# Kernel tuning notes

Hardware: AMD Instinct MI355X
Metric: run time of the kernel (lower is better)

Reference implementation:

```python
import jax, jax.numpy as jnp
import numpy as np

B, S, D = 2, 2048, 1024
H = 16
HD = D // H
MLP = 4096
EPS = 1e-5


def _layernorm(x, g, b):
    mu = jnp.mean(x, axis=-1, keepdims=True)
    var = jnp.mean(jnp.square(x - mu), axis=-1, keepdims=True)
    return (x - mu) * jax.lax.rsqrt(var + EPS) * g + b


def setup_inputs() -> dict:
    key = jax.random.key(0)
    ks = jax.random.split(key, 16)
    sd = 0.02
    return {
        "x": jax.random.normal(ks[0], (B, S, D), jnp.float32),
        "dis_attn_mask": jax.random.normal(ks[1], (B, S, S), jnp.float32) * 0.1,
        "cls_attn_mask": jax.random.normal(ks[2], (B, S, S), jnp.float32) * 0.1,
        "wq": jax.random.normal(ks[3], (D, D), jnp.float32) * sd,
        "bq": jnp.zeros((D,), jnp.float32),
        "wk": jax.random.normal(ks[4], (D, D), jnp.float32) * sd,
        "bk": jnp.zeros((D,), jnp.float32),
        "wv": jax.random.normal(ks[5], (D, D), jnp.float32) * sd,
        "bv": jnp.zeros((D,), jnp.float32),
        "ln1_g": jnp.ones((D,), jnp.float32),
        "ln1_b": jnp.zeros((D,), jnp.float32),
        "ln2_g": jnp.ones((D,), jnp.float32),
        "ln2_b": jnp.zeros((D,), jnp.float32),
        "w1": jax.random.normal(ks[6], (D, MLP), jnp.float32) * sd,
        "b1": jnp.zeros((MLP,), jnp.float32),
        "w2": jax.random.normal(ks[7], (MLP, D), jnp.float32) * sd,
        "b2": jnp.zeros((D,), jnp.float32),
    }


def reference(x, dis_attn_mask, cls_attn_mask, wq, bq, wk, bk, wv, bv,
              ln1_g, ln1_b, ln2_g, ln2_b, w1, b1, w2, b2):
    res = x
    h = _layernorm(x, ln1_g, ln1_b)
    q = h @ wq + bq
    k = h @ wk + bk
    v = h @ wv + bv
    # NOTE: original torch code uses .view(B, H, S, HD) on a contiguous
    # [B, S, D] tensor (no transpose); row-major reshape reproduces this.
    q = q.reshape(B, H, S, HD)
    k = k.reshape(B, H, S, HD)
    v = v.reshape(B, H, S, HD)
    w = jnp.einsum('bhsd,bhtd->bhst', q, k) * (HD ** -0.5)
    w = w + dis_attn_mask[:, None] + cls_attn_mask[:, None]
    w = jax.nn.softmax(w, axis=-1)
    h_attn = jnp.einsum('bhst,bhtd->bhsd', w, v).reshape(B, S, D)
    h = h_attn + res
    h = _layernorm(h, ln2_g, ln2_b)
    res2 = h
    h = jax.nn.gelu(h @ w1 + b1, approximate=False) @ w2 + b2
    return h + res2
```

## Files before the change

### kernel.cpp

```cpp
#include <hip/hip_runtime.h>
#include <hip/hip_bf16.h>
#include <math.h>

#define BB 2
#define SS 2048
#define DD 1024
#define HH 16
#define MLPD 4096

typedef __attribute__((ext_vector_type(8))) short bf16x8;
typedef __attribute__((ext_vector_type(4))) float f32x4;
typedef __attribute__((ext_vector_type(4))) unsigned short us4;

static __device__ __forceinline__ float fast_exp2(float x) {
#if __has_builtin(__builtin_amdgcn_exp2f)
  return __builtin_amdgcn_exp2f(x);
#else
  return exp2f(x);
#endif
}
static __device__ __forceinline__ float fast_rcp(float x) {
#if __has_builtin(__builtin_amdgcn_rcpf)
  return __builtin_amdgcn_rcpf(x);
#else
  return 1.0f / x;
#endif
}

static __device__ __forceinline__ unsigned short f2bf(float f) {
  union { float f; unsigned int u; } v; v.f = f;
  unsigned int r = v.u + 0x7fffu + ((v.u >> 16) & 1u);
  return (unsigned short)(r >> 16);
}
static __device__ __forceinline__ float bf2f(unsigned short b) {
  return __uint_as_float(((unsigned int)b) << 16);
}

static __device__ __forceinline__ float gelu_f(float x) {
  float u = x * x;
  float z = x * fmaf(u, 0.0713548162f, 1.59576912f);
  float e = fast_exp2(z * -1.44269504f);
  return x * fast_rcp(1.0f + e);
}

static __device__ __forceinline__ int swz(int row) {
  return (row & 3) ^ ((row >> 2) & 3);
}

static __device__ __forceinline__ void async16(const unsigned short* g, unsigned short* l) {
  __builtin_amdgcn_global_load_lds(
      (const __attribute__((address_space(1))) unsigned int*)g,
      (__attribute__((address_space(3))) unsigned int*)l, 16, 0, 0);
}

__global__ __launch_bounds__(256) void transpose_to_bf16(
    const float* __restrict__ src, unsigned short* __restrict__ dst,
    int K, int N) {
  __shared__ float tile[32][33];
  int t = threadIdx.x;
  int c = t & 31, rl = t >> 5;
  int bx = blockIdx.x, by = blockIdx.y;
#pragma unroll
  for (int i = 0; i < 4; ++i) {
    int row = rl * 4 + i;
    tile[row][c] = src[(size_t)(by * 32 + row) * N + bx * 32 + c];
  }
  __syncthreads();
#pragma unroll
  for (int i = 0; i < 4; ++i) {
    int n = rl * 4 + i;
    dst[(size_t)(bx * 32 + n) * K + by * 32 + c] = f2bf(tile[c][n]);
  }
}

__global__ __launch_bounds__(256) void transpose_qkv(
    const float* __restrict__ wq, const float* __restrict__ wk,
    const float* __restrict__ wv, unsigned short* __restrict__ dst) {
  __shared__ float tile[32][33];
  const float* src = blockIdx.z == 0 ? wq : blockIdx.z == 1 ? wk : wv;
  unsigned short* d = dst + (size_t)blockIdx.z * 1024 * 1024;
  int t = threadIdx.x;
  int c = t & 31, rl = t >> 5;
  int bx = blockIdx.x, by = blockIdx.y;
#pragma unroll
  for (int i = 0; i < 4; ++i) {
    int row = rl * 4 + i;
    tile[row][c] = src[(size_t)(by * 32 + row) * DD + bx * 32 + c];
  }
  __syncthreads();
#pragma unroll
  for (int i = 0; i < 4; ++i) {
    int n = rl * 4 + i;
    d[(size_t)(bx * 32 + n) * DD + by * 32 + c] = f2bf(tile[c][n]);
  }
}

__global__ __launch_bounds__(256) void concat_bias(
    const float* __restrict__ bq, const float* __restrict__ bk,
    const float* __restrict__ bv, float* __restrict__ dst) {
  int i = blockIdx.x * 256 + threadIdx.x;
  if (i < 1024) dst[i] = bq[i];
  else if (i < 2048) dst[i] = bk[i - 1024];
  else if (i < 3072) dst[i] = bv[i - 2048];
}

__global__ __launch_bounds__(256) void mask_prep3(
    const float* __restrict__ dis, const float* __restrict__ cls,
    unsigned short* __restrict__ cmP) {
  __shared__ unsigned short sm[16][512];
  int qtO = blockIdx.x, waveO = blockIdx.y;
  int b = blockIdx.z >> 2, ktg = blockIdx.z & 3;
  int t = threadIdx.x;
  int row0 = qtO * 128 + waveO * 16;
  int col0 = ktg * 512;
  const float* db = dis + (size_t)b * SS * SS;
  const float* cb = cls + (size_t)b * SS * SS;
  int lrow = t >> 4, lcg = t & 15;
#pragma unroll
  for (int shot = 0; shot < 8; ++shot) {
    int cc = lcg * 4 + shot * 64;
    size_t idx = (size_t)(row0 + lrow) * SS + col0 + cc;
    float4 d4 = *(const float4*)(db + idx);
    float4 c4 = *(const float4*)(cb + idx);
    us4 o;
    o[0] = f2bf((d4.x + c4.x) * 8.0f);
    o[1] = f2bf((d4.y + c4.y) * 8.0f);
    o[2] = f2bf((d4.z + c4.z) * 8.0f);
    o[3] = f2bf((d4.w + c4.w) * 8.0f);
    *(us4*)&sm[lrow][cc] = o;
  }
  __syncthreads();
  int ktL = t >> 5, lp = t & 31;
  unsigned short* ob =
      cmP + ((((size_t)b * 16 + qtO) * 8 + waveO) * 32 + ktg * 8 + ktL) * 64 * 16;
#pragma unroll
  for (int li = 0; li < 2; ++li) {
    int l = lp * 2 + li;
    int g = l >> 4, c16 = l & 15;
    short v[16];
#pragma unroll
    for (int t4 = 0; t4 < 4; ++t4)
#pragma unroll
      for (int r = 0; r < 4; ++r)
        v[t4 * 4 + r] = (short)sm[g * 4 + r][ktL * 64 + t4 * 16 + c16];
    unsigned short* o = ob + (size_t)l * 16;
    *(bf16x8*)(o) = *(bf16x8*)&v[0];
    *(bf16x8*)(o + 8) = *(bf16x8*)&v[8];
  }
}

template <bool BF_IN, bool ADD>
__global__ __launch_bounds__(256) void ln_bf16(
    const void* __restrict__ in, const float* __restrict__ add,
    const float* __restrict__ g, const float* __restrict__ beta,
    unsigned short* __restrict__ out) {
  int row = blockIdx.x;
  int t = threadIdx.x;
  float x[4];
  if (BF_IN) {
    us4 b4 = *(const us4*)((const unsigned short*)in + (size_t)row * DD + t * 4);
#pragma unroll
    for (int i = 0; i < 4; ++i) x[i] = bf2f(b4[i]);
  } else {
    float4 f4 = *(const float4*)((const float*)in + (size_t)row * DD + t * 4);
    x[0] = f4.x; x[1] = f4.y; x[2] = f4.z; x[3] = f4.w;
  }
  if (ADD) {
    float4 a4 = *(const float4*)(add + (size_t)row * DD + t * 4);
    x[0] += a4.x; x[1] += a4.y; x[2] += a4.z; x[3] += a4.w;
  }
  float s1 = x[0] + x[1] + x[2] + x[3];
  float s2 = x[0] * x[0] + x[1] * x[1] + x[2] * x[2] + x[3] * x[3];
#pragma unroll
  for (int off = 32; off > 0; off >>= 1) {
    s1 += __shfl_down(s1, off);
    s2 += __shfl_down(s2, off);
  }
  __shared__ float sa[4], sb[4];
  int wid = t >> 6;
  if ((t & 63) == 0) { sa[wid] = s1; sb[wid] = s2; }
  __syncthreads();
  s1 = sa[0] + sa[1] + sa[2] + sa[3];
  s2 = sb[0] + sb[1] + sb[2] + sb[3];
  float mean = s1 * (1.0f / 1024.0f);
  float var = s2 * (1.0f / 1024.0f) - mean * mean;
  float rstd = rsqrtf(var + 1e-5f);
  float4 gv = *(const float4*)(g + t * 4);
  float4 bv = *(const float4*)(beta + t * 4);
  us4 o;
  o[0] = f2bf((x[0] - mean) * rstd * gv.x + bv.x);
  o[1] = f2bf((x[1] - mean) * rstd * gv.y + bv.y);
  o[2] = f2bf((x[2] - mean) * rstd * gv.z + bv.z);
  o[3] = f2bf((x[3] - mean) * rstd * gv.w + bv.w);
  *(us4*)(out + (size_t)row * DD + t * 4) = o;
}

template <int BN, bool GELU, bool ADDSRC, bool OUT_BF16, bool SPLIT3>
__global__ __launch_bounds__(256) void gemm_bf16(
    const unsigned short* __restrict__ A, const unsigned short* __restrict__ BT,
    const float* __restrict__ bias, const unsigned short* __restrict__ addsrc,
    void* C0, void* C1, void* C2, int M, int N, int K) {
  constexpr int BJ = BN / 32;
  constexpr int BCH = BN / 64;
  __shared__ __align__(16) unsigned short As[128][32];
  __shared__ __align__(16) unsigned short Bs[BN][32];
  int tid = threadIdx.x;
  int wave = tid >> 6, lane = tid & 63;
  int g = lane >> 4, c16 = lane & 15;
  int nwg = gridDim.x * gridDim.y;
  int wg = blockIdx.y * gridDim.x + blockIdx.x;
  int cpx = nwg >> 3;
  int sw = (wg & 7) * cpx + (wg >> 3);
  int bxs = sw % gridDim.x, bys = sw / gridDim.x;
  int m0 = bys * 128, n0 = bxs * BN;
  int wm = (wave >> 1) * 64, wn = (wave & 1) * (BN / 2);
  int lrow = lane >> 2, lq = lane & 3;
  int dq = (lq ^ swz(lrow)) * 8;
  const unsigned short* aS = A + (size_t)(m0 + wave * 32 + lrow) * K + lq * 8;
  unsigned short* aD0 = &As[wave * 32 + lrow][dq];
  unsigned short* aD1 = &As[wave * 32 + 16 + lrow][dq];
  const unsigned short* bS = BT + (size_t)(n0 + wave * (BCH * 16) + lrow) * K + lq * 8;
  unsigned short* bD0 = &Bs[wave * (BCH * 16) + lrow][dq];
  unsigned short* bD1 = &Bs[(wave * (BCH * 16) + 16 + lrow) % BN][dq];
  int vA = (g ^ swz(c16)) * 8;
  const int KI = K / 32;
  const size_t rK = 16 * (size_t)K;

  bf16x8 a0a = *(const bf16x8*)(aS);
  bf16x8 a1a = *(const bf16x8*)(aS + rK);
  bf16x8 b0a = *(const bf16x8*)(bS);
  bf16x8 b1a;
  if constexpr (BCH == 2) b1a = *(const bf16x8*)(bS + rK);
  bf16x8 a0b = *(const bf16x8*)(aS + 32);
  bf16x8 a1b = *(const bf16x8*)(aS + rK + 32);
  bf16x8 b0b = *(const bf16x8*)(bS + 32);
  bf16x8 b1b;
  if constexpr (BCH == 2) b1b = *(const bf16x8*)(bS + rK + 32);

  f32x4 acc[4][BJ] = {};
  for (int kt = 0; kt < KI; kt += 2) {
    __syncthreads();
    *(bf16x8*)aD0 = a0a;
    *(bf16x8*)aD1 = a1a;
    *(bf16x8*)bD0 = b0a;
    if constexpr (BCH == 2) *(bf16x8*)bD1 = b1a;
    __syncthreads();
    if (kt + 2 < KI) {
      int ko = (kt + 2) * 32;
      a0a = *(const bf16x8*)(aS + ko);
      a1a = *(const bf16x8*)(aS + rK + ko);
      b0a = *(const bf16x8*)(bS + ko);
      if constexpr (BCH == 2) b1a = *(const bf16x8*)(bS + rK + ko);
    }
    {
      bf16x8 a[4], b[BJ];
#pragma unroll
      for (int i = 0; i < 4; ++i) a[i] = *(const bf16x8*)&As[wm + i * 16 + c16][vA];
#pragma unroll
      for (int j = 0; j < BJ; ++j) b[j] = *(const bf16x8*)&Bs[wn + j * 16 + c16][vA];
#pragma unroll
      for (int i = 0; i < 4; ++i)
#pragma unroll
        for (int j = 0; j < BJ; ++j)
          acc[i][j] = __builtin_amdgcn_mfma_f32_16x16x32_bf16(a[i], b[j], acc[i][j], 0, 0, 0);
    }
    __syncthreads();
    *(bf16x8*)aD0 = a0b;
    *(bf16x8*)aD1 = a1b;
    *(bf16x8*)bD0 = b0b;
    if constexpr (BCH == 2) *(bf16x8*)bD1 = b1b;
    __syncthreads();
    if (kt + 3 < KI) {
      int ko = (kt + 3) * 32;
      a0b = *(const bf16x8*)(aS + ko);
      a1b = *(const bf16x8*)(aS + rK + ko);
      b0b = *(const bf16x8*)(bS + ko);
      if constexpr (BCH == 2) b1b = *(const bf16x8*)(bS + rK + ko);
    }
    {
      bf16x8 a[4], b[BJ];
#pragma unroll
      for (int i = 0; i < 4; ++i) a[i] = *(const bf16x8*)&As[wm + i * 16 + c16][vA];
#pragma unroll
      for (int j = 0; j < BJ; ++j) b[j] = *(const bf16x8*)&Bs[wn + j * 16 + c16][vA];
#pragma unroll
      for (int i = 0; i < 4; ++i)
#pragma unroll
        for (int j = 0; j < BJ; ++j)
          acc[i][j] = __builtin_amdgcn_mfma_f32_16x16x32_bf16(a[i], b[j], acc[i][j], 0, 0, 0);
    }
  }
  unsigned short* dstb = nullptr;
  int lc0 = 0;
  if (SPLIT3) {
    int which = n0 >> 10;
    dstb = (unsigned short*)(which == 0 ? C0 : which == 1 ? C1 : C2);
    lc0 = n0 & 1023;
  }
#pragma unroll
  for (int j = 0; j < BJ; ++j) {
    int coff = wn + j * 16 + c16;
    float bj = bias[n0 + coff];
#pragma unroll
    for (int i = 0; i < 4; ++i) {
#pragma unroll
      for (int r = 0; r < 4; ++r) {
        int row = m0 + wm + i * 16 + g * 4 + r;
        float cval = acc[i][j][r] + bj;
        if (GELU) cval = gelu_f(cval);
        if (ADDSRC) cval += bf2f(addsrc[(size_t)row * N + n0 + coff]);
        if (SPLIT3) {
          dstb[(size_t)row * 1024 + lc0 + coff] = f2bf(cval);
        } else if (OUT_BF16) {
          ((unsigned short*)C0)[(size_t)row * N + n0 + coff] = f2bf(cval);
        } else {
          ((float*)C0)[(size_t)row * N + n0 + coff] = cval;
        }
      }
    }
  }
}

#define VMW(n) asm volatile("s_waitcnt vmcnt(" #n ")" ::: "memory")
#define BARX() do { asm volatile("" ::: "memory"); \
                    __builtin_amdgcn_s_barrier(); \
                    asm volatile("" ::: "memory"); } while (0)

template <bool GELU, bool SPLIT3>
__global__ __launch_bounds__(512, 2) void gemm256(
    const unsigned short* __restrict__ A, const unsigned short* __restrict__ BT,
    const float* __restrict__ bias, void* C0, void* C1, void* C2,
    int N, int K) {
  __shared__ __align__(16) char lds[2][2][2][16384];
  int tid = threadIdx.x;
  int lane = tid & 63, w = tid >> 6;
  int g = lane >> 4, c16 = lane & 15;
  int wm16 = (w >> 2) << 4;
  int wn16 = (w & 3) << 4;
  int nwg = gridDim.x * gridDim.y;
  int wg = blockIdx.y * gridDim.x + blockIdx.x;
  int cpx = nwg >> 3;
  int sw = (wg & 7) * cpx + (wg >> 3);
  int bx = sw % gridDim.x, by = sw / gridDim.x;
  int m0 = by << 8, n0 = bx << 8;

  int st0 = tid >> 6, ci0 = tid & 63;
  int cp0 = ci0 ^ (((ci0 >> 5) & 1) << 1);
  int sr0 = ((st0 >> 1) << 4) + (cp0 >> 2);
  int sk0 = ((st0 & 1) << 5) + ((cp0 & 3) << 3);
  size_t soff = (size_t)sr0 * K + sk0;

  auto stage = [&](int op, int h, int tt, int d) {
    const unsigned short* base = (op == 0 ? A : BT);
    int row0 = (op == 0 ? m0 : n0) + (h << 7);
    const unsigned short* src = base + (size_t)row0 * K + (tt << 6) + soff;
    unsigned short* dst = (unsigned short*)&lds[op][d][h][tid * 16];
    async16(src, dst);
    async16(src + ((size_t)K << 6), dst + 4096);
  };

  auto foff = [&](int r, int ke) -> int {
    int stt = ((r >> 4) << 1) + (ke >> 5);
    int loc = ((r & 15) << 6) + ((ke & 31) << 1);
    return (stt << 10) + (loc ^ (((r >> 3) & 1) << 5));
  };
  int offA[4][2], offB[2][2];
#pragma unroll
  for (int ii = 0; ii < 4; ++ii)
#pragma unroll
    for (int ks = 0; ks < 2; ++ks)
      offA[ii][ks] = foff(ii * 32 + wm16 + c16, ks * 32 + g * 8);
#pragma unroll
  for (int jj = 0; jj < 2; ++jj)
#pragma unroll
    for (int ks = 0; ks < 2; ++ks)
      offB[jj][ks] = foff(jj * 64 + wn16 + c16, ks * 32 + g * 8);

  f32x4 acc[8][4] = {};

#define MFMA_Q(IH, JH, AF, BF) do {                                           \
    __builtin_amdgcn_s_setprio(1);                                            \
    _Pragma("unroll") for (int ii = 0; ii < 4; ++ii)                          \
      _Pragma("unroll") for (int jj = 0; jj < 2; ++jj) {                      \
        acc[(IH)*4+ii][(JH)*2+jj] = __builtin_amdgcn_mfma_f32_16x16x32_bf16(  \
            AF[ii][0], BF[jj][0], acc[(IH)*4+ii][(JH)*2+jj], 0, 0, 0);        \
        acc[(IH)*4+ii][(JH)*2+jj] = __builtin_amdgcn_mfma_f32_16x16x32_bf16(  \
            AF[ii][1], BF[jj][1], acc[(IH)*4+ii][(JH)*2+jj], 0, 0, 0);        \
      }                                                                       \
    __builtin_amdgcn_s_setprio(0);                                            \
  } while (0)

  stage(0, 0, 0, 0);
  stage(1, 0, 0, 0);
  stage(0, 1, 0, 0);
  stage(1, 1, 0, 0);
  VMW(4);
  BARX();

  const int KT = K >> 6;
  for (int kt = 0; kt < KT; ++kt) {
    int d = kt & 1, dn = d ^ 1;
    int t1 = kt + 1 < KT ? kt + 1 : KT - 1;
    const char* pd = &lds[0][d][0][0];
    bf16x8 A0f[4][2], A1f[4][2], Bf[2][2];

#pragma unroll
    for (int ii = 0; ii < 4; ++ii)
#pragma unroll
      for (int ks = 0; ks < 2; ++ks)
        A0f[ii][ks] = *(const bf16x8*)(pd + offA[ii][ks]);
#pragma unroll
    for (int jj = 0; jj < 2; ++jj)
#pragma unroll
      for (int ks = 0; ks < 2; ++ks)
        Bf[jj][ks] = *(const bf16x8*)(pd + 65536 + offB[jj][ks]);
    stage(0, 0, t1, dn);
    stage(1, 0, t1, dn);
    VMW(6);
    BARX();
    MFMA_Q(0, 0, A0f, Bf);
    BARX();

#pragma unroll
    for (int ii = 0; ii < 4; ++ii)
#pragma unroll
      for (int ks = 0; ks < 2; ++ks)
        A1f[ii][ks] = *(const bf16x8*)(pd + 16384 + offA[ii][ks]);
    stage(0, 1, t1, dn);
    VMW(6);
    BARX();
    MFMA_Q(1, 0, A1f, Bf);
    BARX();

#pragma unroll
    for (int jj = 0; jj < 2; ++jj)
#pragma unroll
      for (int ks = 0; ks < 2; ++ks)
        Bf[jj][ks] = *(const bf16x8*)(pd + 81920 + offB[jj][ks]);
    stage(1, 1, t1, dn);
    BARX();
    MFMA_Q(1, 1, A1f, Bf);
    BARX();

    VMW(4);
    BARX();
    MFMA_Q(0, 1, A0f, Bf);
    BARX();
  }
#undef MFMA_Q
  VMW(0);

  unsigned short* dstb = nullptr;
  int lc0 = 0;
  if (SPLIT3) {
    int which = n0 >> 10;
    dstb = (unsigned short*)(which == 0 ? C0 : which == 1 ? C1 : C2);
    lc0 = n0 & 1023;
  }
#pragma unroll
  for (int i = 0; i < 8; ++i) {
#pragma unroll
    for (int j = 0; j < 4; ++j) {
      int row_b = m0 + ((i >> 2) << 7) + ((i & 3) << 5) + wm16 + (g << 2);
      int colp = ((j >> 1) << 7) + ((j & 1) << 6) + wn16 + c16;
      float bj = bias[n0 + colp];
#pragma unroll
      for (int r = 0; r < 4; ++r) {
        float cv = acc[i][j][r] + bj;
        if (GELU) cv = gelu_f(cv);
        int row = row_b + r;
        if (SPLIT3) {
          dstb[(size_t)row * 1024 + lc0 + colp] = f2bf(cv);
        } else {
          ((unsigned short*)C0)[(size_t)row * N + n0 + colp] = f2bf(cv);
        }
      }
    }
  }
}

__global__ __launch_bounds__(512) void attn_mfma256(
    const unsigned short* __restrict__ q, const unsigned short* __restrict__ k,
    const unsigned short* __restrict__ v, const unsigned short* __restrict__ cmP,
    unsigned short* __restrict__ outO) {
  __shared__ __align__(16) unsigned short Ks[2][64][32];
  __shared__ __align__(16) unsigned short Vt[64][72];
  __shared__ __align__(16) unsigned short Ps[256][72];
  int tid = threadIdx.x;
  int wave = tid >> 6, lane = tid & 63;
  int g = lane >> 4, c16 = lane & 15;
  int w = blockIdx.x + 8 * blockIdx.y + 128 * blockIdx.z;
  int qt = (w >> 4) & 7;
  int b = (w >> 3) & 1;
  int h = (w & 7) | (((w >> 7) & 1) << 3);
  int s0 = qt * 256;
  int wr = wave * 32;
  size_t headoff = (size_t)b * SS * DD + (size_t)h * SS * 64;
  const unsigned short* qb = q + headoff;
  const unsigned short* kb = k + headoff;
  const unsigned short* vb = v + headoff;
  int qtA = qt * 2 + (wave >> 2);
  int wOA = (wave & 3) * 2;
  const unsigned short* csrcA =
      cmP + ((((size_t)b * 16 + qtA) * 8 + wOA) * 2048 + lane) * 16;
  const unsigned short* csrcB = csrcA + 2048 * 16;

  int kkey = tid >> 3, kseg = tid & 7;
  unsigned short* kdst = &Ks[kseg >> 2][kkey][((kseg & 3) ^ swz(kkey)) * 8];
  const unsigned short* ksrc = kb + (size_t)kkey * 64 + kseg * 8;
  const unsigned short* vsrc = vb + (size_t)lane * 64 + wave * 8;
  int vK = (g ^ swz(c16)) * 8;

  bf16x8 qf0A, qf1A, qf0B, qf1B;
  {
    size_t qrowA = (size_t)(s0 + wr + c16) * 64;
    size_t qrowB = (size_t)(s0 + wr + 16 + c16) * 64;
    qf0A = *(const bf16x8*)(qb + qrowA + g * 8);
    qf1A = *(const bf16x8*)(qb + qrowA + 32 + g * 8);
    qf0B = *(const bf16x8*)(qb + qrowB + g * 8);
    qf1B = *(const bf16x8*)(qb + qrowB + 32 + g * 8);
  }
  bf16x8 ones;
#pragma unroll
  for (int j = 0; j < 8; ++j) ones[j] = (short)0x3F80;
  f32x4 oA[4] = {}, oB[4] = {};
  f32x4 olA = {}, olB = {};
  const float scale2 = 0.18033688f;

  bf16x8 kreg = *(const bf16x8*)(ksrc);
  bf16x8 vreg = *(const bf16x8*)(vsrc);
  bf16x8 cmA0 = *(const bf16x8*)(csrcA);
  bf16x8 cmA1 = *(const bf16x8*)(csrcA + 8);
  bf16x8 cmB0 = *(const bf16x8*)(csrcB);
  bf16x8 cmB1 = *(const bf16x8*)(csrcB + 8);

  for (int kt = 0; kt < 32; ++kt) {
    __syncthreads();
    *(bf16x8*)kdst = kreg;
#pragma unroll
    for (int j = 0; j < 8; ++j) Vt[wave * 8 + j][lane] = (unsigned short)vreg[j];
    __syncthreads();

    int ktn = kt + 1 < 32 ? kt + 1 : 31;
    bf16x8 kregN = *(const bf16x8*)(ksrc + (size_t)ktn * 4096);
    bf16x8 vregN = *(const bf16x8*)(vsrc + (size_t)ktn * 4096);
    bf16x8 cmA0N = *(const bf16x8*)(csrcA + (size_t)ktn * 1024);
    bf16x8 cmA1N = *(const bf16x8*)(csrcA + (size_t)ktn * 1024 + 8);
    bf16x8 cmB0N = *(const bf16x8*)(csrcB + (size_t)ktn * 1024);
    bf16x8 cmB1N = *(const bf16x8*)(csrcB + (size_t)ktn * 1024 + 8);

    f32x4 sA[4], sB[4];
#pragma unroll
    for (int r = 0; r < 4; ++r) {
      sA[0][r] = bf2f((unsigned short)cmA0[r]);
      sA[1][r] = bf2f((unsigned short)cmA0[4 + r]);
      sA[2][r] = bf2f((unsigned short)cmA1[r]);
      sA[3][r] = bf2f((unsigned short)cmA1[4 + r]);
      sB[0][r] = bf2f((unsigned short)cmB0[r]);
      sB[1][r] = bf2f((unsigned short)cmB0[4 + r]);
      sB[2][r] = bf2f((unsigned short)cmB1[r]);
      sB[3][r] = bf2f((unsigned short)cmB1[4 + r]);
    }
#pragma unroll
    for (int t = 0; t < 4; ++t) {
      bf16x8 b0 = *(const bf16x8*)&Ks[0][t * 16 + c16][vK];
      bf16x8 b1 = *(const bf16x8*)&Ks[1][t * 16 + c16][vK];
      sA[t] = __builtin_amdgcn_mfma_f32_16x16x32_bf16(qf0A, b0, sA[t], 0, 0, 0);
      sA[t] = __builtin_amdgcn_mfma_f32_16x16x32_bf16(qf1A, b1, sA[t], 0, 0, 0);
      sB[t] = __builtin_amdgcn_mfma_f32_16x16x32_bf16(qf0B, b0, sB[t], 0, 0, 0);
      sB[t] = __builtin_amdgcn_mfma_f32_16x16x32_bf16(qf1B, b1, sB[t], 0, 0, 0);
    }
#pragma unroll
    for (int t = 0; t < 4; ++t) {
      int colw = ((t + g) & 3) * 16 + c16;
#pragma unroll
      for (int r = 0; r < 4; ++r) {
        float pA = fast_exp2(sA[t][r] * scale2);
        Ps[wr + g * 4 + r][colw] = (unsigned short)(__float_as_uint(pA) >> 16);
        float pB = fast_exp2(sB[t][r] * scale2);
        Ps[wr + 16 + g * 4 + r][colw] = (unsigned short)(__float_as_uint(pB) >> 16);
      }
    }
#pragma unroll
    for (int ks = 0; ks < 2; ++ks) {
      int ttc = ((ks * 2 + (g >> 1)) + ((c16 >> 2) & 3)) & 3;
      int colp = ttc * 16 + (g & 1) * 8;
      bf16x8 paA = *(const bf16x8*)&Ps[wr + c16][colp];
      bf16x8 paB = *(const bf16x8*)&Ps[wr + 16 + c16][colp];
#pragma unroll
      for (int t2 = 0; t2 < 4; ++t2) {
        bf16x8 vb8 = *(const bf16x8*)&Vt[t2 * 16 + c16][ks * 32 + g * 8];
        oA[t2] = __builtin_amdgcn_mfma_f32_16x16x32_bf16(paA, vb8, oA[t2], 0, 0, 0);
        oB[t2] = __builtin_amdgcn_mfma_f32_16x16x32_bf16(paB, vb8, oB[t2], 0, 0, 0);
      }
      olA = __builtin_amdgcn_mfma_f32_16x16x32_bf16(paA, ones, olA, 0, 0, 0);
      olB = __builtin_amdgcn_mfma_f32_16x16x32_bf16(paB, ones, olB, 0, 0, 0);
    }
    kreg = kregN;
    vreg = vregN;
    cmA0 = cmA0N; cmA1 = cmA1N;
    cmB0 = cmB0N; cmB1 = cmB1N;
  }
  float invA[4], invB[4];
#pragma unroll
  for (int r = 0; r < 4; ++r) {
    invA[r] = fast_rcp(olA[r]);
    invB[r] = fast_rcp(olB[r]);
  }
#pragma unroll
  for (int t2 = 0; t2 < 4; ++t2)
#pragma unroll
    for (int r = 0; r < 4; ++r) {
      int srowA = s0 + wr + g * 4 + r;
      int srowB = srowA + 16;
      outO[headoff + (size_t)srowA * 64 + t2 * 16 + c16] = f2bf(oA[t2][r] * invA[r]);
      outO[headoff + (size_t)srowB * 64 + t2 * 16 + c16] = f2bf(oB[t2][r] * invB[r]);
    }
}

extern "C" void kernel_launch(void* const* d_in, const int* in_sizes, int n_in,
                              void* d_out, int out_size, void* d_ws, size_t ws_size,
                              hipStream_t stream) {
  const float* x    = (const float*)d_in[0];
  const float* dis  = (const float*)d_in[1];
  const float* cls  = (const float*)d_in[2];
  const float* wq   = (const float*)d_in[3];
  const float* bq   = (const float*)d_in[4];
  const float* wk   = (const float*)d_in[5];
  const float* bk   = (const float*)d_in[6];
  const float* wv   = (const float*)d_in[7];
  const float* bv   = (const float*)d_in[8];
  const float* ln1g = (const float*)d_in[9];
  const float* ln1b = (const float*)d_in[10];
  const float* ln2g = (const float*)d_in[11];
  const float* ln2b = (const float*)d_in[12];
  const float* w1   = (const float*)d_in[13];
  const float* b1   = (const float*)d_in[14];
  const float* w2   = (const float*)d_in[15];
  const float* b2   = (const float*)d_in[16];
  float* out = (float*)d_out;
  char* ws = (char*)d_ws;

  unsigned short* qkvwT = (unsigned short*)(ws + 0);
  unsigned short* w1T   = (unsigned short*)(ws + 6291456);
  unsigned short* w2T   = (unsigned short*)(ws + 14680064);
  float*          qkvb  = (float*)(ws + 23068672);
  unsigned short* r1    = (unsigned short*)(ws + 23134208);
  unsigned short* qbuf  = (unsigned short*)(ws + 31522816);
  unsigned short* kbuf  = (unsigned short*)(ws + 39911424);
  unsigned short* vbuf  = (unsigned short*)(ws + 48300032);
  unsigned short* h2    = (unsigned short*)(ws + 56688640);
  unsigned short* cmP   = (unsigned short*)(ws + 65077248);
  unsigned short* mm    = (unsigned short*)(ws + 23134208);
  unsigned short* h1 = r1;
  unsigned short* attnO = r1;

  const int rows = BB * SS;

  transpose_qkv<<<dim3(DD / 32, DD / 32, 3), 256, 0, stream>>>(wq, wk, wv, qkvwT);
  transpose_to_bf16<<<dim3(MLPD / 32, DD / 32), 256, 0, stream>>>(w1, w1T, DD, MLPD);
  transpose_to_bf16<<<dim3(DD / 32, MLPD / 32), 256, 0, stream>>>(w2, w2T, MLPD, DD);
  concat_bias<<<12, 256, 0, stream>>>(bq, bk, bv, qkvb);
  mask_prep3<<<dim3(16, 8, 8), 256, 0, stream>>>(dis, cls, cmP);

  ln_bf16<false, false><<<rows, 256, 0, stream>>>(x, nullptr, ln1g, ln1b, h1);

  gemm256<false, true><<<dim3(3072 / 256, rows / 256), 512, 0, stream>>>(
      h1, qkvwT, qkvb, qbuf, kbuf, vbuf, 3072, DD);

  attn_mfma256<<<dim3(SS / 256, HH, BB), 512, 0, stream>>>(
      qbuf, kbuf, vbuf, cmP, attnO);

  ln_bf16<true, true><<<rows, 256, 0, stream>>>(attnO, x, ln2g, ln2b, h2);

  gemm256<true, false><<<dim3(MLPD / 256, rows / 256), 512, 0, stream>>>(
      h2, w1T, b1, mm, nullptr, nullptr, MLPD, DD);

  gemm_bf16<64, false, true, false, false><<<dim3(DD / 64, rows / 128), 256, 0, stream>>>(
      mm, w2T, b2, h2, out, nullptr, nullptr, rows, DD, MLPD);
}
```

Measured before the change: 388.4 us.

## Fuse prep kernels into one launch and keep attention P in registers

Merges LN1, the three weight transposes, bias concat and mask packing into a single prep_all launch to cut launch overhead and let independent work overlap. The attention kernel is rewritten to compute S transposed (K as the A operand), so exp results stay in registers and feed the PV MFMA directly, removing the Ps shared-memory round trip. Blocks shrink to 256 threads with 128 query rows each, and the mask layout is adjusted to match. Outputs are written as vectorized us4 stores. Risks are register pressure and a changed V/mask layout that must line up exactly with the new MFMA fragment mapping.

```diff
diff --git a/kernel.cpp b/kernel.cpp
--- a/kernel.cpp
+++ b/kernel.cpp
@@ -35,6 +35,9 @@
 static __device__ __forceinline__ float bf2f(unsigned short b) {
   return __uint_as_float(((unsigned int)b) << 16);
 }
+static __device__ __forceinline__ unsigned int packbf(float lo, float hi) {
+  return (__float_as_uint(lo) >> 16) | (__float_as_uint(hi) & 0xFFFF0000u);
+}
 
 static __device__ __forceinline__ float gelu_f(float x) {
   float u = x * x;
@@ -53,99 +56,147 @@
       (__attribute__((address_space(3))) unsigned int*)l, 16, 0, 0);
 }
 
-__global__ __launch_bounds__(256) void transpose_to_bf16(
-    const float* __restrict__ src, unsigned short* __restrict__ dst,
-    int K, int N) {
-  __shared__ float tile[32][33];
+__global__ __launch_bounds__(256) void prep_all(
+    const float* __restrict__ x, const float* __restrict__ ln1g,
+    const float* __restrict__ ln1b, unsigned short* __restrict__ h1,
+    const float* __restrict__ wq, const float* __restrict__ wk,
+    const float* __restrict__ wv, unsigned short* __restrict__ qkvwT,
+    const float* __restrict__ w1, unsigned short* __restrict__ w1T,
+    const float* __restrict__ w2, unsigned short* __restrict__ w2T,
+    const float* __restrict__ dis, const float* __restrict__ cls,
+    unsigned short* __restrict__ cmP,
+    const float* __restrict__ bq, const float* __restrict__ bk,
+    const float* __restrict__ bv, float* __restrict__ qkvb) {
+  __shared__ __align__(16) char smraw[16384];
+  int bid = blockIdx.x;
   int t = threadIdx.x;
-  int c = t & 31, rl = t >> 5;
-  int bx = blockIdx.x, by = blockIdx.y;
-#pragma unroll
-  for (int i = 0; i < 4; ++i) {
-    int row = rl * 4 + i;
-    tile[row][c] = src[(size_t)(by * 32 + row) * N + bx * 32 + c];
-  }
-  __syncthreads();
-#pragma unroll
-  for (int i = 0; i < 4; ++i) {
-    int n = rl * 4 + i;
-    dst[(size_t)(bx * 32 + n) * K + by * 32 + c] = f2bf(tile[c][n]);
-  }
-}
-
-__global__ __launch_bounds__(256) void transpose_qkv(
-    const float* __restrict__ wq, const float* __restrict__ wk,
-    const float* __restrict__ wv, unsigned short* __restrict__ dst) {
-  __shared__ float tile[32][33];
-  const float* src = blockIdx.z == 0 ? wq : blockIdx.z == 1 ? wk : wv;
-  unsigned short* d = dst + (size_t)blockIdx.z * 1024 * 1024;
-  int t = threadIdx.x;
-  int c = t & 31, rl = t >> 5;
-  int bx = blockIdx.x, by = blockIdx.y;
-#pragma unroll
-  for (int i = 0; i < 4; ++i) {
-    int row = rl * 4 + i;
-    tile[row][c] = src[(size_t)(by * 32 + row) * DD + bx * 32 + c];
-  }
-  __syncthreads();
-#pragma unroll
-  for (int i = 0; i < 4; ++i) {
-    int n = rl * 4 + i;
-    d[(size_t)(bx * 32 + n) * DD + by * 32 + c] = f2bf(tile[c][n]);
-  }
-}
-
-__global__ __launch_bounds__(256) void concat_bias(
-    const float* __restrict__ bq, const float* __restrict__ bk,
-    const float* __restrict__ bv, float* __restrict__ dst) {
-  int i = blockIdx.x * 256 + threadIdx.x;
-  if (i < 1024) dst[i] = bq[i];
-  else if (i < 2048) dst[i] = bk[i - 1024];
-  else if (i < 3072) dst[i] = bv[i - 2048];
-}
-
-__global__ __launch_bounds__(256) void mask_prep3(
-    const float* __restrict__ dis, const float* __restrict__ cls,
-    unsigned short* __restrict__ cmP) {
-  __shared__ unsigned short sm[16][512];
-  int qtO = blockIdx.x, waveO = blockIdx.y;
-  int b = blockIdx.z >> 2, ktg = blockIdx.z & 3;
-  int t = threadIdx.x;
-  int row0 = qtO * 128 + waveO * 16;
-  int col0 = ktg * 512;
-  const float* db = dis + (size_t)b * SS * SS;
-  const float* cb = cls + (size_t)b * SS * SS;
-  int lrow = t >> 4, lcg = t & 15;
-#pragma unroll
-  for (int shot = 0; shot < 8; ++shot) {
-    int cc = lcg * 4 + shot * 64;
-    size_t idx = (size_t)(row0 + lrow) * SS + col0 + cc;
-    float4 d4 = *(const float4*)(db + idx);
-    float4 c4 = *(const float4*)(cb + idx);
+  if (bid < 4096) {
+    int row = bid;
+    float xv[4];
+    float4 f4 = *(const float4*)(x + (size_t)row * DD + t * 4);
+    xv[0] = f4.x; xv[1] = f4.y; xv[2] = f4.z; xv[3] = f4.w;
+    float s1 = xv[0] + xv[1] + xv[2] + xv[3];
+    float s2 = xv[0]*xv[0] + xv[1]*xv[1] + xv[2]*xv[2] + xv[3]*xv[3];
+#pragma unroll
+    for (int off = 32; off > 0; off >>= 1) {
+      s1 += __shfl_down(s1, off);
+      s2 += __shfl_down(s2, off);
+    }
+    float* sa = (float*)smraw;
+    float* sb = sa + 8;
+    int wid = t >> 6;
+    if ((t & 63) == 0) { sa[wid] = s1; sb[wid] = s2; }
+    __syncthreads();
+    s1 = sa[0] + sa[1] + sa[2] + sa[3];
+    s2 = sb[0] + sb[1] + sb[2] + sb[3];
+    float mean = s1 * (1.0f / 1024.0f);
+    float var = s2 * (1.0f / 1024.0f) - mean * mean;
+    float rstd = rsqrtf(var + 1e-5f);
+    float4 gv = *(const float4*)(ln1g + t * 4);
+    float4 bv4 = *(const float4*)(ln1b + t * 4);
     us4 o;
-    o[0] = f2bf((d4.x + c4.x) * 8.0f);
-    o[1] = f2bf((d4.y + c4.y) * 8.0f);
-    o[2] = f2bf((d4.z + c4.z) * 8.0f);
-    o[3] = f2bf((d4.w + c4.w) * 8.0f);
-    *(us4*)&sm[lrow][cc] = o;
-  }
-  __syncthreads();
-  int ktL = t >> 5, lp = t & 31;
-  unsigned short* ob =
-      cmP + ((((size_t)b * 16 + qtO) * 8 + waveO) * 32 + ktg * 8 + ktL) * 64 * 16;
-#pragma unroll
-  for (int li = 0; li < 2; ++li) {
-    int l = lp * 2 + li;
-    int g = l >> 4, c16 = l & 15;
-    short v[16];
-#pragma unroll
-    for (int t4 = 0; t4 < 4; ++t4)
-#pragma unroll
-      for (int r = 0; r < 4; ++r)
-        v[t4 * 4 + r] = (short)sm[g * 4 + r][ktL * 64 + t4 * 16 + c16];
-    unsigned short* o = ob + (size_t)l * 16;
-    *(bf16x8*)(o) = *(bf16x8*)&v[0];
-    *(bf16x8*)(o + 8) = *(bf16x8*)&v[8];
+    o[0] = f2bf((xv[0] - mean) * rstd * gv.x + bv4.x);
+    o[1] = f2bf((xv[1] - mean) * rstd * gv.y + bv4.y);
+    o[2] = f2bf((xv[2] - mean) * rstd * gv.z + bv4.z);
+    o[3] = f2bf((xv[3] - mean) * rstd * gv.w + bv4.w);
+    *(us4*)(h1 + (size_t)row * DD + t * 4) = o;
+  } else if (bid < 4096 + 3072) {
+    int id = bid - 4096;
+    int z = id >> 10;
+    int rem = id & 1023;
+    int bx = rem & 31, by = rem >> 5;
+    const float* src = z == 0 ? wq : z == 1 ? wk : wv;
+    unsigned short* d = qkvwT + (size_t)z * 1024 * 1024;
+    float (*tile)[33] = (float (*)[33])smraw;
+    int c = t & 31, rl = t >> 5;
+#pragma unroll
+    for (int i = 0; i < 4; ++i) {
+      int row = rl * 4 + i;
+      tile[row][c] = src[(size_t)(by * 32 + row) * DD + bx * 32 + c];
+    }
+    __syncthreads();
+#pragma unroll
+    for (int i = 0; i < 4; ++i) {
+      int n = rl * 4 + i;
+      d[(size_t)(bx * 32 + n) * DD + by * 32 + c] = f2bf(tile[c][n]);
+    }
+  } else if (bid < 4096 + 3072 + 4096) {
+    int id = bid - (4096 + 3072);
+    int bx = id & 127, by = id >> 7;
+    float (*tile)[33] = (float (*)[33])smraw;
+    int c = t & 31, rl = t >> 5;
+#pragma unroll
+    for (int i = 0; i < 4; ++i) {
+      int row = rl * 4 + i;
+      tile[row][c] = w1[(size_t)(by * 32 + row) * MLPD + bx * 32 + c];
+    }
+    __syncthreads();
+#pragma unroll
+    for (int i = 0; i < 4; ++i) {
+      int n = rl * 4 + i;
+      w1T[(size_t)(bx * 32 + n) * DD + by * 32 + c] = f2bf(tile[c][n]);
+    }
+  } else if (bid < 4096 + 3072 + 4096 + 4096) {
+    int id = bid - (4096 + 3072 + 4096);
+    int bx = id & 31, by = id >> 5;
+    float (*tile)[33] = (float (*)[33])smraw;
+    int c = t & 31, rl = t >> 5;
+#pragma unroll
+    for (int i = 0; i < 4; ++i) {
+      int row = rl * 4 + i;
+      tile[row][c] = w2[(size_t)(by * 32 + row) * DD + bx * 32 + c];
+    }
+    __syncthreads();
+#pragma unroll
+    for (int i = 0; i < 4; ++i) {
+      int n = rl * 4 + i;
+      w2T[(size_t)(bx * 32 + n) * MLPD + by * 32 + c] = f2bf(tile[c][n]);
+    }
+  } else if (bid < 4096 + 3072 + 4096 + 4096 + 1024) {
+    int id = bid - (4096 + 3072 + 4096 + 4096);
+    int qt16 = id & 127, ktg = (id >> 7) & 3, b = id >> 9;
+    unsigned short (*sm)[512] = (unsigned short (*)[512])smraw;
+    int row0 = qt16 * 16, col0 = ktg * 512;
+    const float* db = dis + (size_t)b * SS * SS;
+    const float* cb = cls + (size_t)b * SS * SS;
+    int lrow = t >> 4, lcg = t & 15;
+#pragma unroll
+    for (int shot = 0; shot < 8; ++shot) {
+      int cc = lcg * 4 + shot * 64;
+      size_t idx = (size_t)(row0 + lrow) * SS + col0 + cc;
+      float4 d4 = *(const float4*)(db + idx);
+      float4 c4 = *(const float4*)(cb + idx);
+      us4 o;
+      o[0] = f2bf((d4.x + c4.x) * 8.0f);
+      o[1] = f2bf((d4.y + c4.y) * 8.0f);
+      o[2] = f2bf((d4.z + c4.z) * 8.0f);
+      o[3] = f2bf((d4.w + c4.w) * 8.0f);
+      *(us4*)&sm[lrow][cc] = o;
+    }
+    __syncthreads();
+    int ktL = t >> 5, lp = t & 31;
+    unsigned short* ob =
+        cmP + (((size_t)(b * 128 + qt16) * 32 + ktg * 8 + ktL) * 64) * 16;
+#pragma unroll
+    for (int li = 0; li < 2; ++li) {
+      int l = lp * 2 + li;
+      int g = l >> 4, c16 = l & 15;
+      short vv[16];
+#pragma unroll
+      for (int ta = 0; ta < 4; ++ta)
+#pragma unroll
+        for (int r = 0; r < 4; ++r)
+          vv[ta * 4 + r] = (short)sm[c16][ktL * 64 + ta * 16 + g * 4 + r];
+      unsigned short* o = ob + (size_t)l * 16;
+      *(bf16x8*)(o) = *(bf16x8*)&vv[0];
+      *(bf16x8*)(o + 8) = *(bf16x8*)&vv[8];
+    }
+  } else {
+    int id = bid - (4096 + 3072 + 4096 + 4096 + 1024);
+    int i = id * 256 + t;
+    if (i < 1024) qkvb[i] = bq[i];
+    else if (i < 2048) qkvb[i] = bk[i - 1024];
+    else if (i < 3072) qkvb[i] = bv[i - 2048];
   }
 }
 
@@ -479,47 +530,41 @@
   }
 }
 
-__global__ __launch_bounds__(512) void attn_mfma256(
+__global__ __launch_bounds__(256) void attn_mfma7(
     const unsigned short* __restrict__ q, const unsigned short* __restrict__ k,
     const unsigned short* __restrict__ v, const unsigned short* __restrict__ cmP,
     unsigned short* __restrict__ outO) {
   __shared__ __align__(16) unsigned short Ks[2][64][32];
   __shared__ __align__(16) unsigned short Vt[64][72];
-  __shared__ __align__(16) unsigned short Ps[256][72];
   int tid = threadIdx.x;
   int wave = tid >> 6, lane = tid & 63;
   int g = lane >> 4, c16 = lane & 15;
-  int w = blockIdx.x + 8 * blockIdx.y + 128 * blockIdx.z;
-  int qt = (w >> 4) & 7;
-  int b = (w >> 3) & 1;
-  int h = (w & 7) | (((w >> 7) & 1) << 3);
-  int s0 = qt * 256;
-  int wr = wave * 32;
+  int h = blockIdx.x, qt = blockIdx.y, b = blockIdx.z;
+  int qbA = qt * 128 + wave * 32;
+  int qbB = qbA + 16;
   size_t headoff = (size_t)b * SS * DD + (size_t)h * SS * 64;
-  const unsigned short* qb = q + headoff;
+  const unsigned short* qp = q + headoff;
   const unsigned short* kb = k + headoff;
   const unsigned short* vb = v + headoff;
-  int qtA = qt * 2 + (wave >> 2);
-  int wOA = (wave & 3) * 2;
+  int qt16A = qbA >> 4;
   const unsigned short* csrcA =
-      cmP + ((((size_t)b * 16 + qtA) * 8 + wOA) * 2048 + lane) * 16;
-  const unsigned short* csrcB = csrcA + 2048 * 16;
-
-  int kkey = tid >> 3, kseg = tid & 7;
-  unsigned short* kdst = &Ks[kseg >> 2][kkey][((kseg & 3) ^ swz(kkey)) * 8];
-  const unsigned short* ksrc = kb + (size_t)kkey * 64 + kseg * 8;
-  const unsigned short* vsrc = vb + (size_t)lane * 64 + wave * 8;
+      cmP + (((size_t)(b * 128 + qt16A) * 32 * 64) + lane) * 16;
+  const unsigned short* csrcB = csrcA + 32 * 64 * 16;
+
+  int kkey = tid >> 2, lq2 = tid & 3;
+  int ksg0 = lq2 * 2, ksg1 = ksg0 + 1;
+  unsigned short* kdst0 = &Ks[ksg0 >> 2][kkey][((ksg0 & 3) ^ swz(kkey)) * 8];
+  unsigned short* kdst1 = &Ks[ksg1 >> 2][kkey][((ksg1 & 3) ^ swz(kkey)) * 8];
+  const unsigned short* ksrc = kb + (size_t)kkey * 64 + ksg0 * 8;
+
+  int vcol = (lane & 0x20) | ((lane & 0x0C) << 1) | ((lane & 0x10) >> 2) | (lane & 3);
+  const unsigned short* vsrc = vb + (size_t)lane * 64 + wave * 16;
   int vK = (g ^ swz(c16)) * 8;
 
-  bf16x8 qf0A, qf1A, qf0B, qf1B;
-  {
-    size_t qrowA = (size_t)(s0 + wr + c16) * 64;
-    size_t qrowB = (size_t)(s0 + wr + 16 + c16) * 64;
-    qf0A = *(const bf16x8*)(qb + qrowA + g * 8);
-    qf1A = *(const bf16x8*)(qb + qrowA + 32 + g * 8);
-    qf0B = *(const bf16x8*)(qb + qrowB + g * 8);
-    qf1B = *(const bf16x8*)(qb + qrowB + 32 + g * 8);
-  }
+  bf16x8 qf0A = *(const bf16x8*)(qp + (size_t)(qbA + c16) * 64 + g * 8);
+  bf16x8 qf1A = *(const bf16x8*)(qp + (size_t)(qbA + c16) * 64 + 32 + g * 8);
+  bf16x8 qf0B = *(const bf16x8*)(qp + (size_t)(qbB + c16) * 64 + g * 8);
+  bf16x8 qf1B = *(const bf16x8*)(qp + (size_t)(qbB + c16) * 64 + 32 + g * 8);
   bf16x8 ones;
 #pragma unroll
   for (int j = 0; j < 8; ++j) ones[j] = (short)0x3F80;
@@ -527,8 +572,10 @@
   f32x4 olA = {}, olB = {};
   const float scale2 = 0.18033688f;
 
-  bf16x8 kreg = *(const bf16x8*)(ksrc);
-  bf16x8 vreg = *(const bf16x8*)(vsrc);
+  bf16x8 kregA = *(const bf16x8*)(ksrc);
+  bf16x8 kregB = *(const bf16x8*)(ksrc + 8);
+  bf16x8 vregA = *(const bf16x8*)(vsrc);
+  bf16x8 vregB = *(const bf16x8*)(vsrc + 8);
   bf16x8 cmA0 = *(const bf16x8*)(csrcA);
   bf16x8 cmA1 = *(const bf16x8*)(csrcA + 8);
   bf16x8 cmB0 = *(const bf16x8*)(csrcB);
@@ -536,14 +583,20 @@
 
   for (int kt = 0; kt < 32; ++kt) {
     __syncthreads();
-    *(bf16x8*)kdst = kreg;
-#pragma unroll
-    for (int j = 0; j < 8; ++j) Vt[wave * 8 + j][lane] = (unsigned short)vreg[j];
+    *(bf16x8*)kdst0 = kregA;
+    *(bf16x8*)kdst1 = kregB;
+#pragma unroll
+    for (int j = 0; j < 8; ++j) {
+      Vt[wave * 16 + j][vcol] = (unsigned short)vregA[j];
+      Vt[wave * 16 + 8 + j][vcol] = (unsigned short)vregB[j];
+    }
     __syncthreads();
 
     int ktn = kt + 1 < 32 ? kt + 1 : 31;
-    bf16x8 kregN = *(const bf16x8*)(ksrc + (size_t)ktn * 4096);
-    bf16x8 vregN = *(const bf16x8*)(vsrc + (size_t)ktn * 4096);
+    bf16x8 kregAN = *(const bf16x8*)(ksrc + (size_t)ktn * 4096);
+    bf16x8 kregBN = *(const bf16x8*)(ksrc + (size_t)ktn * 4096 + 8);
+    bf16x8 vregAN = *(const bf16x8*)(vsrc + (size_t)ktn * 4096);
+    bf16x8 vregBN = *(const bf16x8*)(vsrc + (size_t)ktn * 4096 + 8);
     bf16x8 cmA0N = *(const bf16x8*)(csrcA + (size_t)ktn * 1024);
     bf16x8 cmA1N = *(const bf16x8*)(csrcA + (size_t)ktn * 1024 + 8);
     bf16x8 cmB0N = *(const bf16x8*)(csrcB + (size_t)ktn * 1024);
@@ -562,60 +615,66 @@
       sB[3][r] = bf2f((unsigned short)cmB1[4 + r]);
     }
 #pragma unroll
-    for (int t = 0; t < 4; ++t) {
-      bf16x8 b0 = *(const bf16x8*)&Ks[0][t * 16 + c16][vK];
-      bf16x8 b1 = *(const bf16x8*)&Ks[1][t * 16 + c16][vK];
-      sA[t] = __builtin_amdgcn_mfma_f32_16x16x32_bf16(qf0A, b0, sA[t], 0, 0, 0);
-      sA[t] = __builtin_amdgcn_mfma_f32_16x16x32_bf16(qf1A, b1, sA[t], 0, 0, 0);
-      sB[t] = __builtin_amdgcn_mfma_f32_16x16x32_bf16(qf0B, b0, sB[t], 0, 0, 0);
-      sB[t] = __builtin_amdgcn_mfma_f32_16x16x32_bf16(qf1B, b1, sB[t], 0, 0, 0);
-    }
-#pragma unroll
-    for (int t = 0; t < 4; ++t) {
-      int colw = ((t + g) & 3) * 16 + c16;
+    for (int ta = 0; ta < 4; ++ta) {
+      bf16x8 kf0 = *(const bf16x8*)&Ks[0][ta * 16 + c16][vK];
+      bf16x8 kf1 = *(const bf16x8*)&Ks[1][ta * 16 + c16][vK];
+      sA[ta] = __builtin_amdgcn_mfma_f32_16x16x32_bf16(kf0, qf0A, sA[ta], 0, 0, 0);
+      sA[ta] = __builtin_amdgcn_mfma_f32_16x16x32_bf16(kf1, qf1A, sA[ta], 0, 0, 0);
+      sB[ta] = __builtin_amdgcn_mfma_f32_16x16x32_bf16(kf0, qf0B, sB[ta], 0, 0, 0);
+      sB[ta] = __builtin_amdgcn_mfma_f32_16x16x32_bf16(kf1, qf1B, sB[ta], 0, 0, 0);
+    }
+    float eA[16], eB[16];
+#pragma unroll
+    for (int ta = 0; ta < 4; ++ta)
 #pragma unroll
       for (int r = 0; r < 4; ++r) {
-        float pA = fast_exp2(sA[t][r] * scale2);
-        Ps[wr + g * 4 + r][colw] = (unsigned short)(__float_as_uint(pA) >> 16);
-        float pB = fast_exp2(sB[t][r] * scale2);
-        Ps[wr + 16 + g * 4 + r][colw] = (unsigned short)(__float_as_uint(pB) >> 16);
+        eA[ta * 4 + r] = fast_exp2(sA[ta][r] * scale2);
+        eB[ta * 4 + r] = fast_exp2(sB[ta][r] * scale2);
       }
-    }
+    bf16x8 pbA[2], pbB[2];
 #pragma unroll
     for (int ks = 0; ks < 2; ++ks) {
-      int ttc = ((ks * 2 + (g >> 1)) + ((c16 >> 2) & 3)) & 3;
-      int colp = ttc * 16 + (g & 1) * 8;
-      bf16x8 paA = *(const bf16x8*)&Ps[wr + c16][colp];
-      bf16x8 paB = *(const bf16x8*)&Ps[wr + 16 + c16][colp];
+      union { unsigned int w[4]; bf16x8 v8; } ua, ub;
+      ua.w[0] = packbf(eA[8 * ks + 0], eA[8 * ks + 1]);
+      ua.w[1] = packbf(eA[8 * ks + 2], eA[8 * ks + 3]);
+      ua.w[2] = packbf(eA[8 * ks + 4], eA[8 * ks + 5]);
+      ua.w[3] = packbf(eA[8 * ks + 6], eA[8 * ks + 7]);
+      ub.w[0] = packbf(eB[8 * ks + 0], eB[8 * ks + 1]);
+      ub.w[1] = packbf(eB[8 * ks + 2], eB[8 * ks + 3]);
+      ub.w[2] = packbf(eB[8 * ks + 4], eB[8 * ks + 5]);
+      ub.w[3] = packbf(eB[8 * ks + 6], eB[8 * ks + 7]);
+      pbA[ks] = ua.v8;
+      pbB[ks] = ub.v8;
+    }
+#pragma unroll
+    for (int ks = 0; ks < 2; ++ks) {
 #pragma unroll
       for (int t2 = 0; t2 < 4; ++t2) {
         bf16x8 vb8 = *(const bf16x8*)&Vt[t2 * 16 + c16][ks * 32 + g * 8];
-        oA[t2] = __builtin_amdgcn_mfma_f32_16x16x32_bf16(paA, vb8, oA[t2], 0, 0, 0);
-        oB[t2] = __builtin_amdgcn_mfma_f32_16x16x32_bf16(paB, vb8, oB[t2], 0, 0, 0);
+        oA[t2] = __builtin_amdgcn_mfma_f32_16x16x32_bf16(vb8, pbA[ks], oA[t2], 0, 0, 0);
+        oB[t2] = __builtin_amdgcn_mfma_f32_16x16x32_bf16(vb8, pbB[ks], oB[t2], 0, 0, 0);
       }
-      olA = __builtin_amdgcn_mfma_f32_16x16x32_bf16(paA, ones, olA, 0, 0, 0);
-      olB = __builtin_amdgcn_mfma_f32_16x16x32_bf16(paB, ones, olB, 0, 0, 0);
-    }
-    kreg = kregN;
-    vreg = vregN;
+      olA = __builtin_amdgcn_mfma_f32_16x16x32_bf16(ones, pbA[ks], olA, 0, 0, 0);
+      olB = __builtin_amdgcn_mfma_f32_16x16x32_bf16(ones, pbB[ks], olB, 0, 0, 0);
+    }
+    kregA = kregAN; kregB = kregBN;
+    vregA = vregAN; vregB = vregBN;
     cmA0 = cmA0N; cmA1 = cmA1N;
     cmB0 = cmB0N; cmB1 = cmB1N;
   }
-  float invA[4], invB[4];
-#pragma unroll
-  for (int r = 0; r < 4; ++r) {
-    invA[r] = fast_rcp(olA[r]);
-    invB[r] = fast_rcp(olB[r]);
-  }
-#pragma unroll
-  for (int t2 = 0; t2 < 4; ++t2)
+  float invA = fast_rcp(olA[0]);
+  float invB = fast_rcp(olB[0]);
+#pragma unroll
+  for (int t2 = 0; t2 < 4; ++t2) {
+    us4 wA, wB;
 #pragma unroll
     for (int r = 0; r < 4; ++r) {
-      int srowA = s0 + wr + g * 4 + r;
-      int srowB = srowA + 16;
-      outO[headoff + (size_t)srowA * 64 + t2 * 16 + c16] = f2bf(oA[t2][r] * invA[r]);
-      outO[headoff + (size_t)srowB * 64 + t2 * 16 + c16] = f2bf(oB[t2][r] * invB[r]);
-    }
+      wA[r] = f2bf(oA[t2][r] * invA);
+      wB[r] = f2bf(oB[t2][r] * invB);
+    }
+    *(us4*)(outO + headoff + (size_t)(qbA + c16) * 64 + t2 * 16 + g * 4) = wA;
+    *(us4*)(outO + headoff + (size_t)(qbB + c16) * 64 + t2 * 16 + g * 4) = wB;
+  }
 }
 
 extern "C" void kernel_launch(void* const* d_in, const int* in_sizes, int n_in,
@@ -657,18 +716,14 @@
 
   const int rows = BB * SS;
 
-  transpose_qkv<<<dim3(DD / 32, DD / 32, 3), 256, 0, stream>>>(wq, wk, wv, qkvwT);
-  transpose_to_bf16<<<dim3(MLPD / 32, DD / 32), 256, 0, stream>>>(w1, w1T, DD, MLPD);
-  transpose_to_bf16<<<dim3(DD / 32, MLPD / 32), 256, 0, stream>>>(w2, w2T, MLPD, DD);
-  concat_bias<<<12, 256, 0, stream>>>(bq, bk, bv, qkvb);
-  mask_prep3<<<dim3(16, 8, 8), 256, 0, stream>>>(dis, cls, cmP);
-
-  ln_bf16<false, false><<<rows, 256, 0, stream>>>(x, nullptr, ln1g, ln1b, h1);
+  prep_all<<<16396, 256, 0, stream>>>(
+      x, ln1g, ln1b, h1, wq, wk, wv, qkvwT, w1, w1T, w2, w2T,
+      dis, cls, cmP, bq, bk, bv, qkvb);
 
   gemm256<false, true><<<dim3(3072 / 256, rows / 256), 512, 0, stream>>>(
       h1, qkvwT, qkvb, qbuf, kbuf, vbuf, 3072, DD);
 
-  attn_mfma256<<<dim3(SS / 256, HH, BB), 512, 0, stream>>>(
+  attn_mfma7<<<dim3(HH, SS / 128, BB), 256, 0, stream>>>(
       qbuf, kbuf, vbuf, cmP, attnO);
 
   ln_bf16<true, true><<<rows, 256, 0, stream>>>(attnO, x, ln2g, ln2b, h2);
```

Result: faster. 380.3 us (-2.1%).
